# Optimization experiments

Measured on AMD Instinct MI355X. Metric: run time of the kernel, lower is better.

The kernel has to match this reference:

```python
import jax, jax.numpy as jnp
import numpy as np

B, S = 4, 1024          # sequences, tokens per sequence (equal-length prefill)
T = B * S               # total ragged tokens
H, D = 16, 128          # heads, head_size
HID = H * D             # hidden_size = 2048
THETA = 10000.0


def setup_inputs() -> dict:
    key = jax.random.key(0)
    k0, k1, k2, k3 = jax.random.split(key, 4)
    hidden_states = jax.random.normal(k0, (T, HID), jnp.float32) * 0.02
    # real RoPE tables (PositionRotaryEmbedding.static), [T, D//2]
    inv_freq = 1.0 / (THETA ** (jnp.arange(0, D, 2, dtype=jnp.float32) / D))
    pos = jnp.tile(jnp.arange(S, dtype=jnp.float32), B)  # position resets per sequence
    ang = pos[:, None] * inv_freq[None, :]
    cos, sin = jnp.cos(ang), jnp.sin(ang)
    w_attn = jax.random.normal(k1, (3 * HID, HID), jnp.float32) * 0.02
    b_attn = jax.random.normal(k2, (3 * HID,), jnp.float32) * 0.02
    w_proj = jax.random.normal(k3, (HID, HID), jnp.float32) * 0.02
    cu_seqlens = (jnp.arange(B + 1, dtype=jnp.int32) * S)
    return {"hidden_states": hidden_states, "cos": cos, "sin": sin,
            "w_attn": w_attn, "b_attn": b_attn, "w_proj": w_proj,
            "cu_seqlens": cu_seqlens}


def _rope(x, cos, sin):
    # x: [T, H, D]; cos/sin: [T, D//2]; rotate-half (neox) style
    x1, x2 = jnp.split(x, 2, axis=-1)
    c, s = cos[:, None, :], sin[:, None, :]
    return jnp.concatenate([x1 * c - x2 * s, x2 * c + x1 * s], axis=-1)


def reference(hidden_states, cos, sin, w_attn, b_attn, w_proj, cu_seqlens):
    scale = D ** -0.5
    qkv = hidden_states @ w_attn.T + b_attn          # [T, 3*HID]
    q = qkv[:, :HID].reshape(T, H, D)
    k = qkv[:, HID:2 * HID].reshape(T, H, D)
    v = qkv[:, 2 * HID:].reshape(T, H, D)
    q = _rope(q, cos, sin)
    k = _rope(k, cos, sin)
    # equal-length ragged batch -> [B, S, H, D]; causal flash-attn (prefill path)
    qb = q.reshape(B, S, H, D)
    kb = k.reshape(B, S, H, D)
    vb = v.reshape(B, S, H, D)
    scores = jnp.einsum('bqhd,bkhd->bhqk', qb, kb) * scale
    causal = jnp.tril(jnp.ones((S, S), dtype=bool))
    scores = jnp.where(causal[None, None], scores, jnp.finfo(scores.dtype).min)
    p = jax.nn.softmax(scores, axis=-1)
    o = jnp.einsum('bhqk,bkhd->bqhd', p, vb).reshape(T, HID)
    return o @ w_proj.T                               # c_proj, no bias
```

## Files before the change

kernel.cpp:

```cpp
#include <hip/hip_runtime.h>

typedef __bf16 bf16x8 __attribute__((ext_vector_type(8)));
typedef __bf16 bf16x4 __attribute__((ext_vector_type(4)));
typedef float  f32x4  __attribute__((ext_vector_type(4)));

#define T_TOT 4096
#define SEQ   1024
#define BATCH 4
#define HEADS 16
#define DIM   128
#define HIDN  2048
#define QKVW  6144

__device__ __forceinline__ void gld_lds16(const void* g, void* l) {
  __builtin_amdgcn_global_load_lds(
      (const __attribute__((address_space(1))) unsigned int*)g,
      (__attribute__((address_space(3))) unsigned int*)l, 16, 0, 0);
}

__global__ void f2b_kernel(const float* __restrict__ in, __bf16* __restrict__ out, int n) {
  int i = (blockIdx.x * 256 + threadIdx.x) * 4;
  if (i >= n) return;
  const float4 v = *(const float4*)(in + i);
  bf16x4 o;
  o[0] = (__bf16)v.x; o[1] = (__bf16)v.y; o[2] = (__bf16)v.z; o[3] = (__bf16)v.w;
  *(bf16x4*)(out + i) = o;
}

template<int BIAS, typename OUT_T>
__global__ __launch_bounds__(256, 2) void gemm_wide(
    const __bf16* __restrict__ A, int lda,
    const __bf16* __restrict__ B, int ldb,
    const float* __restrict__ bias,
    OUT_T* __restrict__ C, int ldc, int K, int nby)
{
  __shared__ __bf16 sA[3 * 256 * 32];
  __shared__ __bf16 sB[3 * 128 * 32];
  const int tid = threadIdx.x;
  const int w = tid >> 6, lane = tid & 63;
  const int lq = lane & 15, lg = lane >> 4;
  const int wm = w >> 1, wn = w & 1;

  const int nwg = gridDim.x, cpx = nwg >> 3, bid = blockIdx.x;
  const int wgid = (bid & 7) * cpx + (bid >> 3);
  const int by = wgid % nby, bx = wgid / nby;
  const int bm = by * 256, bn = bx * 128;

  const int srow = tid >> 2;
  const int scol = ((tid & 3) ^ ((srow >> 1) & 3)) * 8;
  const __bf16* gA = A + (size_t)(bm + srow) * lda + scol;
  const __bf16* gB = B + (size_t)(bn + srow) * ldb + scol;
  __bf16* dA = &sA[w * 512];
  __bf16* dB = &sB[w * 512];

  const int NT = K >> 5;

#define STAGE(t, bf) {                                               \
    const __bf16* sa_ = gA + (size_t)(t) * 32;                       \
    gld_lds16(sa_,                      dA + (bf) * 8192);           \
    gld_lds16(sa_ + (size_t) 64 * lda,  dA + (bf) * 8192 + 2048);    \
    gld_lds16(sa_ + (size_t)128 * lda,  dA + (bf) * 8192 + 4096);    \
    gld_lds16(sa_ + (size_t)192 * lda,  dA + (bf) * 8192 + 6144);    \
    const __bf16* sb_ = gB + (size_t)(t) * 32;                       \
    gld_lds16(sb_,                      dB + (bf) * 4096);           \
    gld_lds16(sb_ + (size_t) 64 * ldb,  dB + (bf) * 4096 + 2048); }

  f32x4 acc[8][4] = {};

  const int colo = (lg ^ ((lq >> 1) & 3)) * 8;
  const int offA = (wm * 128 + lq) * 32 + colo;
  const int offB = (wn * 64 + lq) * 32 + colo;

  STAGE(0, 0); STAGE(1, 1);
  asm volatile("s_waitcnt vmcnt(6)" ::: "memory");
  __builtin_amdgcn_s_barrier();
  asm volatile("" ::: "memory");

  bf16x8 a[8], b[4];
  {
    const __bf16* pA = &sA[offA];
    const __bf16* pB = &sB[offB];
#pragma unroll
    for (int m = 0; m < 8; ++m) a[m] = *(const bf16x8*)(pA + m * 512);
#pragma unroll
    for (int n = 0; n < 4; ++n) b[n] = *(const bf16x8*)(pB + n * 512);
  }

  int bcur = 0;
  for (int t = 0; t < NT; ++t) {
    int bstg = bcur + 2; if (bstg >= 3) bstg -= 3;
    const bool st = (t + 2) < NT;
    if (st) STAGE(t + 2, bstg);

    asm volatile("s_waitcnt lgkmcnt(0)" ::: "memory");
    __builtin_amdgcn_sched_barrier(0);
    __builtin_amdgcn_s_setprio(1);
#pragma unroll
    for (int m = 0; m < 8; ++m)
#pragma unroll
      for (int n = 0; n < 4; ++n)
        acc[m][n] = __builtin_amdgcn_mfma_f32_16x16x32_bf16(a[m], b[n], acc[m][n], 0, 0, 0);
    __builtin_amdgcn_s_setprio(0);

    if (t + 1 < NT) {
      if (st) { asm volatile("s_waitcnt vmcnt(6)" ::: "memory"); }
      else    { asm volatile("s_waitcnt vmcnt(0)" ::: "memory"); }
      __builtin_amdgcn_s_barrier();
      asm volatile("" ::: "memory");
      const int bnext = (bcur + 1 == 3) ? 0 : bcur + 1;
      const __bf16* pA = &sA[bnext * 8192 + offA];
      const __bf16* pB = &sB[bnext * 4096 + offB];
#pragma unroll
      for (int m = 0; m < 8; ++m) a[m] = *(const bf16x8*)(pA + m * 512);
#pragma unroll
      for (int n = 0; n < 4; ++n) b[n] = *(const bf16x8*)(pB + n * 512);
    }
    bcur = (bcur + 1 == 3) ? 0 : bcur + 1;
  }
#undef STAGE

#pragma unroll
  for (int n = 0; n < 4; ++n) {
    const int col = bn + wn * 64 + n * 16 + lq;
    const float bv = BIAS ? bias[col] : 0.0f;
#pragma unroll
    for (int m = 0; m < 8; ++m)
#pragma unroll
      for (int r = 0; r < 4; ++r) {
        const int row = bm + wm * 128 + m * 16 + lg * 4 + r;
        C[(size_t)row * ldc + col] = (OUT_T)(acc[m][n][r] + bv);
      }
  }
}

template<int BIAS, typename OUT_T>
__global__ __launch_bounds__(512, 4) void gemm_pl(
    const __bf16* __restrict__ A, int lda,
    const __bf16* __restrict__ B, int ldb,
    const float* __restrict__ bias,
    OUT_T* __restrict__ C, int ldc, int K, int nby)
{
  __shared__ __bf16 sA[3 * 128 * 32];
  __shared__ __bf16 sB[3 * 256 * 32];
  const int tid = threadIdx.x;
  const int w = tid >> 6, lane = tid & 63;
  const int lq = lane & 15, lg = lane >> 4;
  const int wm = w >> 2, wn = w & 3;

  const int nwg = gridDim.x;
  const int cpx = nwg >> 3;
  const int bid = blockIdx.x;
  const int wgid = (bid & 7) * cpx + (bid >> 3);
  const int by = wgid % nby, bx = wgid / nby;
  const int bm = by * 128, bn = bx * 256;

  const int srow = tid >> 2;
  const int scol = ((tid & 3) ^ ((srow >> 1) & 3)) * 8;
  const __bf16* gA = A + (size_t)(bm + srow) * lda + scol;
  const __bf16* gB = B + (size_t)(bn + srow) * ldb + scol;
  const size_t strB = (size_t)128 * ldb;
  __bf16* dA = &sA[w * 512];
  __bf16* dB = &sB[w * 512];

  const int NT = K >> 5;

#define STAGE(t, bf) {                                              \
    gld_lds16(gA + (size_t)(t) * 32, dA + (bf) * 4096);             \
    const __bf16* sb_ = gB + (size_t)(t) * 32;                      \
    gld_lds16(sb_, dB + (bf) * 8192);                               \
    gld_lds16(sb_ + strB, dB + (bf) * 8192 + 4096); }

  f32x4 acc[4][4] = {};

  const int colo = (lg ^ ((lq >> 1) & 3)) * 8;
  const int offA = (wm * 64 + lq) * 32 + colo;
  const int offB = (wn * 64 + lq) * 32 + colo;

  STAGE(0, 0); STAGE(1, 1);
  asm volatile("s_waitcnt vmcnt(3)" ::: "memory");
  __builtin_amdgcn_s_barrier();
  asm volatile("" ::: "memory");

  bf16x8 a[4], b[4];
  {
    const __bf16* pA = &sA[offA];
    const __bf16* pB = &sB[offB];
#pragma unroll
    for (int m = 0; m < 4; ++m) a[m] = *(const bf16x8*)(pA + m * 512);
#pragma unroll
    for (int n = 0; n < 4; ++n) b[n] = *(const bf16x8*)(pB + n * 512);
  }

  int bcur = 0;
  for (int t = 0; t < NT; ++t) {
    int bstg = bcur + 2; if (bstg >= 3) bstg -= 3;
    const bool st = (t + 2) < NT;
    if (st) STAGE(t + 2, bstg);

    asm volatile("s_waitcnt lgkmcnt(0)" ::: "memory");
    __builtin_amdgcn_sched_barrier(0);
    __builtin_amdgcn_s_setprio(1);
#pragma unroll
    for (int m = 0; m < 4; ++m)
#pragma unroll
      for (int n = 0; n < 4; ++n)
        acc[m][n] = __builtin_amdgcn_mfma_f32_16x16x32_bf16(a[m], b[n], acc[m][n], 0, 0, 0);
    __builtin_amdgcn_s_setprio(0);

    if (t + 1 < NT) {
      if (st) { asm volatile("s_waitcnt vmcnt(3)" ::: "memory"); }
      else    { asm volatile("s_waitcnt vmcnt(0)" ::: "memory"); }
      __builtin_amdgcn_s_barrier();
      asm volatile("" ::: "memory");
      const int bnext = (bcur + 1 == 3) ? 0 : bcur + 1;
      const __bf16* pA = &sA[bnext * 4096 + offA];
      const __bf16* pB = &sB[bnext * 8192 + offB];
#pragma unroll
      for (int m = 0; m < 4; ++m) a[m] = *(const bf16x8*)(pA + m * 512);
#pragma unroll
      for (int n = 0; n < 4; ++n) b[n] = *(const bf16x8*)(pB + n * 512);
    }
    bcur = (bcur + 1 == 3) ? 0 : bcur + 1;
  }
#undef STAGE

#pragma unroll
  for (int n = 0; n < 4; ++n) {
    const int col = bn + wn * 64 + n * 16 + lq;
    const float bv = BIAS ? bias[col] : 0.0f;
#pragma unroll
    for (int m = 0; m < 4; ++m)
#pragma unroll
      for (int r = 0; r < 4; ++r) {
        const int row = bm + wm * 64 + m * 16 + lg * 4 + r;
        C[(size_t)row * ldc + col] = (OUT_T)(acc[m][n][r] + bv);
      }
  }
}

__global__ __launch_bounds__(256) void pack_kernel(const __bf16* __restrict__ qkv,
                                                   const float* __restrict__ cosb,
                                                   const float* __restrict__ sinb,
                                                   __bf16* __restrict__ Qp,
                                                   __bf16* __restrict__ Kp,
                                                   __bf16* __restrict__ Vt)
{
  __shared__ __bf16 tile[64][136];
  const int bh = blockIdx.y, b = bh >> 4, h = bh & 15;
  const int s0 = blockIdx.x * 64;
  const int tid = threadIdx.x;
  const int j0 = (tid & 7) * 8;
  const float qsc = 0.08838834764831845f;

#pragma unroll
  for (int it = 0; it < 2; ++it) {
    const int r = (tid >> 3) + it * 32;
    const int s = s0 + r;
    const size_t t = (size_t)b * SEQ + s;
    float cc[8], ss[8];
    *(float4*)&cc[0] = *(const float4*)&cosb[t * 64 + j0];
    *(float4*)&cc[4] = *(const float4*)&cosb[t * 64 + j0 + 4];
    *(float4*)&ss[0] = *(const float4*)&sinb[t * 64 + j0];
    *(float4*)&ss[4] = *(const float4*)&sinb[t * 64 + j0 + 4];
    const __bf16* src = qkv + t * QKVW + h * DIM;
    const bf16x8 q1 = *(const bf16x8*)(src + j0);
    const bf16x8 q2 = *(const bf16x8*)(src + 64 + j0);
    const bf16x8 k1 = *(const bf16x8*)(src + HIDN + j0);
    const bf16x8 k2 = *(const bf16x8*)(src + HIDN + 64 + j0);
    bf16x8 oq1, oq2, ok1, ok2;
#pragma unroll
    for (int jj = 0; jj < 8; ++jj) {
      const float c = cc[jj], sn = ss[jj];
      const float a1 = (float)q1[jj], a2 = (float)q2[jj];
      const float b1 = (float)k1[jj], b2 = (float)k2[jj];
      oq1[jj] = (__bf16)((a1 * c - a2 * sn) * qsc);
      oq2[jj] = (__bf16)((a2 * c + a1 * sn) * qsc);
      ok1[jj] = (__bf16)(b1 * c - b2 * sn);
      ok2[jj] = (__bf16)(b2 * c + b1 * sn);
    }
    __bf16* dq = Qp + ((size_t)bh * SEQ + s) * DIM + j0;
    __bf16* dk = Kp + ((size_t)bh * SEQ + s) * DIM + j0;
    *(bf16x8*)dq = oq1; *(bf16x8*)(dq + 64) = oq2;
    *(bf16x8*)dk = ok1; *(bf16x8*)(dk + 64) = ok2;
  }

#pragma unroll
  for (int i = 0; i < 4; ++i) {
    const int r = (tid >> 4) + i * 16;
    const int c = (tid & 15) * 8;
    *(bf16x8*)&tile[r][c] =
        *(const bf16x8*)&qkv[((size_t)b * SEQ + s0 + r) * QKVW + 2 * HIDN + h * DIM + c];
  }
  __syncthreads();
#pragma unroll
  for (int i = 0; i < 4; ++i) {
    const int d = (tid >> 3) + i * 32;
    const int scc = (tid & 7) * 8;
    bf16x8 v;
#pragma unroll
    for (int jj = 0; jj < 8; ++jj) v[jj] = tile[scc + jj][d];
    *(bf16x8*)&Vt[((size_t)bh * DIM + d) * SEQ + s0 + scc] = v;
  }
}

__global__ __launch_bounds__(256, 2) void attn_kernel(const __bf16* __restrict__ Qp,
                                                      const __bf16* __restrict__ Kp,
                                                      const __bf16* __restrict__ Vt,
                                                      __bf16* __restrict__ O)
{
  __shared__ __bf16 sK[2][64 * 128];
  __shared__ __bf16 sV[2][128 * 64];
  __shared__ __bf16 sP[4][32 * 64];
  const int w = threadIdx.x >> 6, lane = threadIdx.x & 63;
  const int lq = lane & 15, lg = lane >> 4;
  const int bh = blockIdx.y, b = bh >> 4, h = bh & 15;
  const int qb = ((int)blockIdx.x + bh) & 7;
  const int q0 = qb * 128 + w * 32;
  const int NTb = 2 * qb + 2;
  const int kend = q0 + 32;

  const __bf16* Qh = Qp + (size_t)bh * SEQ * DIM;
  const __bf16* Kh = Kp + (size_t)bh * SEQ * DIM;
  const __bf16* Vh = Vt + (size_t)bh * DIM * SEQ;

  const int krow = lane >> 4;
  const int kgr  = lane & 15;
  const int vrow = lane >> 3;
  const int vgr  = lane & 7;
  const __bf16* Vsrc = Vh + (size_t)(w * 32 + vrow) * SEQ + (vgr ^ vrow) * 8;

  auto ASTAGE = [&](int ktn, int p) {
#pragma unroll
    for (int i = 0; i < 4; ++i) {
      const int rb = w * 16 + i * 4;
      gld_lds16(Kh + (size_t)(ktn + rb + krow) * DIM + (kgr ^ (i * 4 + krow)) * 8,
                &sK[p][rb * DIM]);
    }
#pragma unroll
    for (int i = 0; i < 4; ++i) {
      gld_lds16(Vsrc + (size_t)i * 8 * SEQ + ktn, &sV[p][(w * 32 + i * 8) * 64]);
    }
  };

  bf16x8 aq[2][4];
#pragma unroll
  for (int m = 0; m < 2; ++m)
#pragma unroll
    for (int kk = 0; kk < 4; ++kk)
      aq[m][kk] = *(const bf16x8*)(Qh + (size_t)(q0 + m * 16 + lq) * DIM + kk * 32 + lg * 8);

  f32x4 accO[2][8] = {};
  float mrow[2][4], lrow[2][4];
#pragma unroll
  for (int m = 0; m < 2; ++m)
#pragma unroll
    for (int r = 0; r < 4; ++r) { mrow[m][r] = -1e30f; lrow[m][r] = 0.0f; }

  ASTAGE(0, 0);
  asm volatile("s_waitcnt vmcnt(0)" ::: "memory");
  __builtin_amdgcn_s_barrier();

  int p = 0;
  for (int t = 0; t < NTb; ++t) {
    const int kt = t * 64;
    if (t + 1 < NTb) ASTAGE(kt + 64, p ^ 1);

    if (kt < kend) {
      f32x4 s[2][4] = {};
#pragma unroll
      for (int n = 0; n < 4; ++n) {
        const int rowb = (n * 16 + lq) * DIM;
#pragma unroll
        for (int kk = 0; kk < 4; ++kk) {
          const bf16x8 bk = *(const bf16x8*)&sK[p][rowb + ((4 * kk + lg) ^ lq) * 8];
#pragma unroll
          for (int m = 0; m < 2; ++m)
            s[m][n] = __builtin_amdgcn_mfma_f32_16x16x32_bf16(aq[m][kk], bk, s[m][n], 0, 0, 0);
        }
      }
      if (kt + 63 > q0) {
#pragma unroll
        for (int n = 0; n < 4; ++n) {
          const int kpos = kt + n * 16 + lq;
#pragma unroll
          for (int m = 0; m < 2; ++m)
#pragma unroll
            for (int r = 0; r < 4; ++r)
              if (kpos > q0 + m * 16 + lg * 4 + r) s[m][n][r] = -1e30f;
        }
      }
#pragma unroll
      for (int m = 0; m < 2; ++m) {
#pragma unroll
        for (int r = 0; r < 4; ++r) {
          float mx = fmaxf(fmaxf(s[m][0][r], s[m][1][r]), fmaxf(s[m][2][r], s[m][3][r]));
          mx = fmaxf(mx, __shfl_xor(mx, 1));
          mx = fmaxf(mx, __shfl_xor(mx, 2));
          mx = fmaxf(mx, __shfl_xor(mx, 4));
          mx = fmaxf(mx, __shfl_xor(mx, 8));
          const float mnew = fmaxf(mrow[m][r], mx);
          const float alpha = __expf(mrow[m][r] - mnew);
          mrow[m][r] = mnew;
          float rs = 0.0f;
#pragma unroll
          for (int n = 0; n < 4; ++n) {
            const float pv = __expf(s[m][n][r] - mnew);
            s[m][n][r] = pv;
            rs += pv;
          }
          rs += __shfl_xor(rs, 1); rs += __shfl_xor(rs, 2);
          rs += __shfl_xor(rs, 4); rs += __shfl_xor(rs, 8);
          lrow[m][r] = lrow[m][r] * alpha + rs;
#pragma unroll
          for (int f = 0; f < 8; ++f) accO[m][f][r] *= alpha;
        }
      }
#pragma unroll
      for (int m = 0; m < 2; ++m)
#pragma unroll
        for (int n = 0; n < 4; ++n)
#pragma unroll
          for (int r = 0; r < 4; ++r) {
            const int prow = m * 16 + lg * 4 + r;
            const int cb = (n * 16 + lq) * 2;
            const int addr = prow * 128 + (((cb >> 4) ^ (prow & 7)) << 4) + (cb & 15);
            *(__bf16*)((char*)&sP[w][0] + addr) = (__bf16)s[m][n][r];
          }
      asm volatile("s_waitcnt lgkmcnt(0)" ::: "memory");
#pragma unroll
      for (int kk2 = 0; kk2 < 2; ++kk2) {
        bf16x8 ap[2];
#pragma unroll
        for (int m = 0; m < 2; ++m) {
          const int prow = m * 16 + lq;
          ap[m] = *(const bf16x8*)((char*)&sP[w][0] +
                   prow * 128 + (((4 * kk2 + lg) ^ (lq & 7)) << 4));
        }
#pragma unroll
        for (int f = 0; f < 8; ++f) {
          const bf16x8 bv = *(const bf16x8*)&sV[p][(f * 16 + lq) * 64 +
                                                   ((4 * kk2 + lg) ^ (lq & 7)) * 8];
#pragma unroll
          for (int m = 0; m < 2; ++m)
            accO[m][f] = __builtin_amdgcn_mfma_f32_16x16x32_bf16(ap[m], bv, accO[m][f], 0, 0, 0);
        }
      }
    }
    asm volatile("s_waitcnt vmcnt(0)" ::: "memory");
    __builtin_amdgcn_s_barrier();
    p ^= 1;
  }

#pragma unroll
  for (int m = 0; m < 2; ++m)
#pragma unroll
    for (int f = 0; f < 8; ++f)
#pragma unroll
      for (int r = 0; r < 4; ++r) {
        const float v = accO[m][f][r] / lrow[m][r];
        O[((size_t)b * SEQ + q0 + m * 16 + lg * 4 + r) * HIDN + h * DIM + f * 16 + lq] = (__bf16)v;
      }
}

extern "C" void kernel_launch(void* const* d_in, const int* in_sizes, int n_in,
                              void* d_out, int out_size, void* d_ws, size_t ws_size,
                              hipStream_t stream)
{
  const float* hidden = (const float*)d_in[0];
  const float* cosb   = (const float*)d_in[1];
  const float* sinb   = (const float*)d_in[2];
  const float* w_attn = (const float*)d_in[3];
  const float* b_attn = (const float*)d_in[4];
  const float* w_proj = (const float*)d_in[5];

  char* ws = (char*)d_ws;
  __bf16* hid_bf   = (__bf16*)(ws);
  __bf16* wattn_bf = (__bf16*)(ws + 16777216);
  __bf16* wproj_bf = (__bf16*)(ws + 41943040);
  __bf16* qkv      = (__bf16*)(ws + 50331648);
  __bf16* Qp       = (__bf16*)(ws);
  __bf16* Kp       = (__bf16*)(ws + 16777216);
  __bf16* Vt       = (__bf16*)(ws + 100663296);
  __bf16* Obuf     = (__bf16*)(ws + 117440512);
  float* out = (float*)d_out;

  f2b_kernel<<<8192, 256, 0, stream>>>(hidden, hid_bf, T_TOT * HIDN);
  f2b_kernel<<<12288, 256, 0, stream>>>(w_attn, wattn_bf, 3 * HIDN * HIDN);
  f2b_kernel<<<4096, 256, 0, stream>>>(w_proj, wproj_bf, HIDN * HIDN);

  gemm_wide<1, __bf16><<<768, 256, 0, stream>>>(
      hid_bf, HIDN, wattn_bf, HIDN, b_attn, qkv, QKVW, HIDN, 16);

  pack_kernel<<<dim3(16, 64), 256, 0, stream>>>(qkv, cosb, sinb, Qp, Kp, Vt);
  attn_kernel<<<dim3(8, 64), 256, 0, stream>>>(Qp, Kp, Vt, Obuf);

  gemm_pl<0, float><<<256, 512, 0, stream>>>(
      Obuf, HIDN, wproj_bf, HIDN, nullptr, out, HIDN, HIDN, 32);
}
```

Baseline: 274.7 us.

## Fuse fp32-to-bf16 casts, double-buffer QKV GEMM, square-tile output projection

Merges the three fp32-to-bf16 conversion launches into a single kernel that dispatches by block index. The QKV GEMM drops from triple to double buffering, which halves its LDS footprint, and raises the occupancy hint to 3 blocks per CU. That buys more resident waves at the cost of a shallower prefetch that waits on vmcnt(0) every iteration. The output projection switches from 512-thread 128x256 tiles to 256-thread 128x128 tiles with 512 blocks, giving finer-grained scheduling across CUs in exchange for more global traffic per output.

Result: slower. 562.8 us (median of 2 runs) (+104.9%).

```diff
diff --git a/kernel.cpp b/kernel.cpp
--- a/kernel.cpp
+++ b/kernel.cpp
@@ -18,9 +18,18 @@
       (__attribute__((address_space(3))) unsigned int*)l, 16, 0, 0);
 }
 
-__global__ void f2b_kernel(const float* __restrict__ in, __bf16* __restrict__ out, int n) {
-  int i = (blockIdx.x * 256 + threadIdx.x) * 4;
-  if (i >= n) return;
+__global__ void f2b_all(const float* __restrict__ h,  __bf16* __restrict__ oh,
+                        const float* __restrict__ wa, __bf16* __restrict__ owa,
+                        const float* __restrict__ wp, __bf16* __restrict__ owp)
+{
+  const int bid = blockIdx.x;
+  const float* in;
+  __bf16* out;
+  int base;
+  if (bid < 8192)       { in = h;  out = oh;  base = bid; }
+  else if (bid < 20480) { in = wa; out = owa; base = bid - 8192; }
+  else                  { in = wp; out = owp; base = bid - 20480; }
+  const int i = (base * 256 + threadIdx.x) * 4;
   const float4 v = *(const float4*)(in + i);
   bf16x4 o;
   o[0] = (__bf16)v.x; o[1] = (__bf16)v.y; o[2] = (__bf16)v.z; o[3] = (__bf16)v.w;
@@ -28,13 +37,112 @@
 }
 
 template<int BIAS, typename OUT_T>
-__global__ __launch_bounds__(256, 2) void gemm_wide(
+__global__ __launch_bounds__(256, 3) void gemm1(
     const __bf16* __restrict__ A, int lda,
     const __bf16* __restrict__ B, int ldb,
     const float* __restrict__ bias,
     OUT_T* __restrict__ C, int ldc, int K, int nby)
 {
-  __shared__ __bf16 sA[3 * 256 * 32];
+  __shared__ __bf16 sA[2 * 256 * 32];
+  __shared__ __bf16 sB[2 * 128 * 32];
+  const int tid = threadIdx.x;
+  const int w = tid >> 6, lane = tid & 63;
+  const int lq = lane & 15, lg = lane >> 4;
+  const int wm = w >> 1, wn = w & 1;
+
+  const int nwg = gridDim.x, cpx = nwg >> 3, bid = blockIdx.x;
+  const int wgid = (bid & 7) * cpx + (bid >> 3);
+  const int by = wgid % nby, bx = wgid / nby;
+  const int bm = by * 256, bn = bx * 128;
+
+  const int srow = tid >> 2;
+  const int scol = ((tid & 3) ^ ((srow >> 1) & 3)) * 8;
+  const __bf16* gA = A + (size_t)(bm + srow) * lda + scol;
+  const __bf16* gB = B + (size_t)(bn + srow) * ldb + scol;
+  const int w16 = w * 16;
+  const int NT = K >> 5;
+
+#define STAGE(t, bf) {                                                    \
+    const __bf16* sa_ = gA + (size_t)(t) * 32;                            \
+    gld_lds16(sa_,                     &sA[(bf) * 8192 + (w16) * 32]);    \
+    gld_lds16(sa_ + (size_t) 64 * lda, &sA[(bf) * 8192 + (64 + w16) * 32]); \
+    gld_lds16(sa_ + (size_t)128 * lda, &sA[(bf) * 8192 + (128 + w16) * 32]); \
+    gld_lds16(sa_ + (size_t)192 * lda, &sA[(bf) * 8192 + (192 + w16) * 32]); \
+    const __bf16* sb_ = gB + (size_t)(t) * 32;                            \
+    gld_lds16(sb_,                     &sB[(bf) * 4096 + (w16) * 32]);    \
+    gld_lds16(sb_ + (size_t) 64 * ldb, &sB[(bf) * 4096 + (64 + w16) * 32]); }
+
+  f32x4 acc[8][4] = {};
+
+  const int colo = (lg ^ ((lq >> 1) & 3)) * 8;
+  const int offA = (wm * 128 + lq) * 32 + colo;
+  const int offB = (wn * 64 + lq) * 32 + colo;
+
+  STAGE(0, 0);
+  asm volatile("s_waitcnt vmcnt(0)" ::: "memory");
+  __builtin_amdgcn_s_barrier();
+  asm volatile("" ::: "memory");
+
+  bf16x8 a[8], b[4];
+  {
+    const __bf16* pA = &sA[offA];
+    const __bf16* pB = &sB[offB];
+#pragma unroll
+    for (int m = 0; m < 8; ++m) a[m] = *(const bf16x8*)(pA + m * 512);
+#pragma unroll
+    for (int n = 0; n < 4; ++n) b[n] = *(const bf16x8*)(pB + n * 512);
+  }
+
+  for (int t = 0; t < NT; ++t) {
+    if (t + 1 < NT) STAGE(t + 1, (t + 1) & 1);
+
+    asm volatile("s_waitcnt lgkmcnt(0)" ::: "memory");
+    __builtin_amdgcn_sched_barrier(0);
+    __builtin_amdgcn_s_setprio(1);
+#pragma unroll
+    for (int m = 0; m < 8; ++m)
+#pragma unroll
+      for (int n = 0; n < 4; ++n)
+        acc[m][n] = __builtin_amdgcn_mfma_f32_16x16x32_bf16(a[m], b[n], acc[m][n], 0, 0, 0);
+    __builtin_amdgcn_s_setprio(0);
+
+    if (t + 1 < NT) {
+      asm volatile("s_waitcnt vmcnt(0)" ::: "memory");
+      __builtin_amdgcn_s_barrier();
+      asm volatile("" ::: "memory");
+      const int bnext = (t + 1) & 1;
+      const __bf16* pA = &sA[bnext * 8192 + offA];
+      const __bf16* pB = &sB[bnext * 4096 + offB];
+#pragma unroll
+      for (int m = 0; m < 8; ++m) a[m] = *(const bf16x8*)(pA + m * 512);
+#pragma unroll
+      for (int n = 0; n < 4; ++n) b[n] = *(const bf16x8*)(pB + n * 512);
+    }
+  }
+#undef STAGE
+
+#pragma unroll
+  for (int n = 0; n < 4; ++n) {
+    const int col = bn + wn * 64 + n * 16 + lq;
+    const float bv = BIAS ? bias[col] : 0.0f;
+#pragma unroll
+    for (int m = 0; m < 8; ++m)
+#pragma unroll
+      for (int r = 0; r < 4; ++r) {
+        const int row = bm + wm * 128 + m * 16 + lg * 4 + r;
+        C[(size_t)row * ldc + col] = (OUT_T)(acc[m][n][r] + bv);
+      }
+  }
+}
+
+template<int BIAS, typename OUT_T>
+__global__ __launch_bounds__(256, 3) void gemm_sq(
+    const __bf16* __restrict__ A, int lda,
+    const __bf16* __restrict__ B, int ldb,
+    const float* __restrict__ bias,
+    OUT_T* __restrict__ C, int ldc, int K, int nby)
+{
+  __shared__ __bf16 sA[3 * 128 * 32];
   __shared__ __bf16 sB[3 * 128 * 32];
   const int tid = threadIdx.x;
   const int w = tid >> 6, lane = tid & 63;
@@ -44,44 +152,40 @@
   const int nwg = gridDim.x, cpx = nwg >> 3, bid = blockIdx.x;
   const int wgid = (bid & 7) * cpx + (bid >> 3);
   const int by = wgid % nby, bx = wgid / nby;
-  const int bm = by * 256, bn = bx * 128;
+  const int bm = by * 128, bn = bx * 128;
 
   const int srow = tid >> 2;
   const int scol = ((tid & 3) ^ ((srow >> 1) & 3)) * 8;
   const __bf16* gA = A + (size_t)(bm + srow) * lda + scol;
   const __bf16* gB = B + (size_t)(bn + srow) * ldb + scol;
-  __bf16* dA = &sA[w * 512];
-  __bf16* dB = &sB[w * 512];
-
+  const int w16 = w * 16;
   const int NT = K >> 5;
 
-#define STAGE(t, bf) {                                               \
-    const __bf16* sa_ = gA + (size_t)(t) * 32;                       \
-    gld_lds16(sa_,                      dA + (bf) * 8192);           \
-    gld_lds16(sa_ + (size_t) 64 * lda,  dA + (bf) * 8192 + 2048);    \
-    gld_lds16(sa_ + (size_t)128 * lda,  dA + (bf) * 8192 + 4096);    \
-    gld_lds16(sa_ + (size_t)192 * lda,  dA + (bf) * 8192 + 6144);    \
-    const __bf16* sb_ = gB + (size_t)(t) * 32;                       \
-    gld_lds16(sb_,                      dB + (bf) * 4096);           \
-    gld_lds16(sb_ + (size_t) 64 * ldb,  dB + (bf) * 4096 + 2048); }
-
-  f32x4 acc[8][4] = {};
+#define STAGE(t, bf) {                                                    \
+    const __bf16* sa_ = gA + (size_t)(t) * 32;                            \
+    gld_lds16(sa_,                     &sA[(bf) * 4096 + (w16) * 32]);    \
+    gld_lds16(sa_ + (size_t)64 * lda,  &sA[(bf) * 4096 + (64 + w16) * 32]); \
+    const __bf16* sb_ = gB + (size_t)(t) * 32;                            \
+    gld_lds16(sb_,                     &sB[(bf) * 4096 + (w16) * 32]);    \
+    gld_lds16(sb_ + (size_t)64 * ldb,  &sB[(bf) * 4096 + (64 + w16) * 32]); }
+
+  f32x4 acc[4][4] = {};
 
   const int colo = (lg ^ ((lq >> 1) & 3)) * 8;
-  const int offA = (wm * 128 + lq) * 32 + colo;
+  const int offA = (wm * 64 + lq) * 32 + colo;
   const int offB = (wn * 64 + lq) * 32 + colo;
 
   STAGE(0, 0); STAGE(1, 1);
-  asm volatile("s_waitcnt vmcnt(6)" ::: "memory");
+  asm volatile("s_waitcnt vmcnt(4)" ::: "memory");
   __builtin_amdgcn_s_barrier();
   asm volatile("" ::: "memory");
 
-  bf16x8 a[8], b[4];
+  bf16x8 a[4], b[4];
   {
     const __bf16* pA = &sA[offA];
     const __bf16* pB = &sB[offB];
 #pragma unroll
-    for (int m = 0; m < 8; ++m) a[m] = *(const bf16x8*)(pA + m * 512);
+    for (int m = 0; m < 4; ++m) a[m] = *(const bf16x8*)(pA + m * 512);
 #pragma unroll
     for (int n = 0; n < 4; ++n) b[n] = *(const bf16x8*)(pB + n * 512);
   }
@@ -96,125 +200,20 @@
     __builtin_amdgcn_sched_barrier(0);
     __builtin_amdgcn_s_setprio(1);
 #pragma unroll
-    for (int m = 0; m < 8; ++m)
+    for (int m = 0; m < 4; ++m)
 #pragma unroll
       for (int n = 0; n < 4; ++n)
         acc[m][n] = __builtin_amdgcn_mfma_f32_16x16x32_bf16(a[m], b[n], acc[m][n], 0, 0, 0);
     __builtin_amdgcn_s_setprio(0);
 
     if (t + 1 < NT) {
-      if (st) { asm volatile("s_waitcnt vmcnt(6)" ::: "memory"); }
-      else    { asm volatile("s_waitcnt vmcnt(0)" ::: "memory"); }
-      __builtin_amdgcn_s_barrier();
-      asm volatile("" ::: "memory");
-      const int bnext = (bcur + 1 == 3) ? 0 : bcur + 1;
-      const __bf16* pA = &sA[bnext * 8192 + offA];
-      const __bf16* pB = &sB[bnext * 4096 + offB];
-#pragma unroll
-      for (int m = 0; m < 8; ++m) a[m] = *(const bf16x8*)(pA + m * 512);
-#pragma unroll
-      for (int n = 0; n < 4; ++n) b[n] = *(const bf16x8*)(pB + n * 512);
-    }
-    bcur = (bcur + 1 == 3) ? 0 : bcur + 1;
-  }
-#undef STAGE
-
-#pragma unroll
-  for (int n = 0; n < 4; ++n) {
-    const int col = bn + wn * 64 + n * 16 + lq;
-    const float bv = BIAS ? bias[col] : 0.0f;
-#pragma unroll
-    for (int m = 0; m < 8; ++m)
-#pragma unroll
-      for (int r = 0; r < 4; ++r) {
-        const int row = bm + wm * 128 + m * 16 + lg * 4 + r;
-        C[(size_t)row * ldc + col] = (OUT_T)(acc[m][n][r] + bv);
-      }
-  }
-}
-
-template<int BIAS, typename OUT_T>
-__global__ __launch_bounds__(512, 4) void gemm_pl(
-    const __bf16* __restrict__ A, int lda,
-    const __bf16* __restrict__ B, int ldb,
-    const float* __restrict__ bias,
-    OUT_T* __restrict__ C, int ldc, int K, int nby)
-{
-  __shared__ __bf16 sA[3 * 128 * 32];
-  __shared__ __bf16 sB[3 * 256 * 32];
-  const int tid = threadIdx.x;
-  const int w = tid >> 6, lane = tid & 63;
-  const int lq = lane & 15, lg = lane >> 4;
-  const int wm = w >> 2, wn = w & 3;
-
-  const int nwg = gridDim.x;
-  const int cpx = nwg >> 3;
-  const int bid = blockIdx.x;
-  const int wgid = (bid & 7) * cpx + (bid >> 3);
-  const int by = wgid % nby, bx = wgid / nby;
-  const int bm = by * 128, bn = bx * 256;
-
-  const int srow = tid >> 2;
-  const int scol = ((tid & 3) ^ ((srow >> 1) & 3)) * 8;
-  const __bf16* gA = A + (size_t)(bm + srow) * lda + scol;
-  const __bf16* gB = B + (size_t)(bn + srow) * ldb + scol;
-  const size_t strB = (size_t)128 * ldb;
-  __bf16* dA = &sA[w * 512];
-  __bf16* dB = &sB[w * 512];
-
-  const int NT = K >> 5;
-
-#define STAGE(t, bf) {                                              \
-    gld_lds16(gA + (size_t)(t) * 32, dA + (bf) * 4096);             \
-    const __bf16* sb_ = gB + (size_t)(t) * 32;                      \
-    gld_lds16(sb_, dB + (bf) * 8192);                               \
-    gld_lds16(sb_ + strB, dB + (bf) * 8192 + 4096); }
-
-  f32x4 acc[4][4] = {};
-
-  const int colo = (lg ^ ((lq >> 1) & 3)) * 8;
-  const int offA = (wm * 64 + lq) * 32 + colo;
-  const int offB = (wn * 64 + lq) * 32 + colo;
-
-  STAGE(0, 0); STAGE(1, 1);
-  asm volatile("s_waitcnt vmcnt(3)" ::: "memory");
-  __builtin_amdgcn_s_barrier();
-  asm volatile("" ::: "memory");
-
-  bf16x8 a[4], b[4];
-  {
-    const __bf16* pA = &sA[offA];
-    const __bf16* pB = &sB[offB];
-#pragma unroll
-    for (int m = 0; m < 4; ++m) a[m] = *(const bf16x8*)(pA + m * 512);
-#pragma unroll
-    for (int n = 0; n < 4; ++n) b[n] = *(const bf16x8*)(pB + n * 512);
-  }
-
-  int bcur = 0;
-  for (int t = 0; t < NT; ++t) {
-    int bstg = bcur + 2; if (bstg >= 3) bstg -= 3;
-    const bool st = (t + 2) < NT;
-    if (st) STAGE(t + 2, bstg);
-
-    asm volatile("s_waitcnt lgkmcnt(0)" ::: "memory");
-    __builtin_amdgcn_sched_barrier(0);
-    __builtin_amdgcn_s_setprio(1);
-#pragma unroll
-    for (int m = 0; m < 4; ++m)
-#pragma unroll
-      for (int n = 0; n < 4; ++n)
-        acc[m][n] = __builtin_amdgcn_mfma_f32_16x16x32_bf16(a[m], b[n], acc[m][n], 0, 0, 0);
-    __builtin_amdgcn_s_setprio(0);
-
-    if (t + 1 < NT) {
-      if (st) { asm volatile("s_waitcnt vmcnt(3)" ::: "memory"); }
+      if (st) { asm volatile("s_waitcnt vmcnt(4)" ::: "memory"); }
       else    { asm volatile("s_waitcnt vmcnt(0)" ::: "memory"); }
       __builtin_amdgcn_s_barrier();
       asm volatile("" ::: "memory");
       const int bnext = (bcur + 1 == 3) ? 0 : bcur + 1;
       const __bf16* pA = &sA[bnext * 4096 + offA];
-      const __bf16* pB = &sB[bnext * 8192 + offB];
+      const __bf16* pB = &sB[bnext * 4096 + offB];
 #pragma unroll
       for (int m = 0; m < 4; ++m) a[m] = *(const bf16x8*)(pA + m * 512);
 #pragma unroll
@@ -484,16 +483,14 @@
   __bf16* Obuf     = (__bf16*)(ws + 117440512);
   float* out = (float*)d_out;
 
-  f2b_kernel<<<8192, 256, 0, stream>>>(hidden, hid_bf, T_TOT * HIDN);
-  f2b_kernel<<<12288, 256, 0, stream>>>(w_attn, wattn_bf, 3 * HIDN * HIDN);
-  f2b_kernel<<<4096, 256, 0, stream>>>(w_proj, wproj_bf, HIDN * HIDN);
-
-  gemm_wide<1, __bf16><<<768, 256, 0, stream>>>(
+  f2b_all<<<24576, 256, 0, stream>>>(hidden, hid_bf, w_attn, wattn_bf, w_proj, wproj_bf);
+
+  gemm1<1, __bf16><<<768, 256, 0, stream>>>(
       hid_bf, HIDN, wattn_bf, HIDN, b_attn, qkv, QKVW, HIDN, 16);
 
   pack_kernel<<<dim3(16, 64), 256, 0, stream>>>(qkv, cosb, sinb, Qp, Kp, Vt);
   attn_kernel<<<dim3(8, 64), 256, 0, stream>>>(Qp, Kp, Vt, Obuf);
 
-  gemm_pl<0, float><<<256, 512, 0, stream>>>(
+  gemm_sq<0, float><<<512, 256, 0, stream>>>(
       Obuf, HIDN, wproj_bf, HIDN, nullptr, out, HIDN, HIDN, 32);
 }
```
